# Kernel tuning notes

Hardware: AMD Instinct MI355X
Metric: run time of the kernel (lower is better)

The kernel has to match this reference:

```python
import jax, jax.numpy as jnp
import numpy as np

N_NODES, N_EDGES = 50000, 800000
NODE_D, EDGE_D, ST_D, HID_D = 64, 32, 32, 128


def _linear_params(key, fan_in, fan_out):
    k1, k2 = jax.random.split(key)
    lim = 1.0 / np.sqrt(fan_in)
    W = jax.random.uniform(k1, (fan_in, fan_out), jnp.float32, -lim, lim)
    b = jax.random.uniform(k2, (fan_out,), jnp.float32, -lim, lim)
    return W, b


def setup_inputs() -> dict:
    key = jax.random.key(0)
    ks = jax.random.split(key, 9)
    node_features = jax.random.normal(ks[0], (N_NODES, NODE_D), jnp.float32)
    edge_features = jax.random.normal(ks[1], (N_EDGES, EDGE_D), jnp.float32)
    spacetime_embeddings = jax.random.normal(ks[2], (N_NODES, ST_D), jnp.float32)
    edge_indices = jax.random.randint(ks[3], (N_EDGES, 2), 0, N_NODES, jnp.int64 if jax.config.jax_enable_x64 else jnp.int32)
    msg_in_d = 2 * NODE_D + EDGE_D + ST_D  # 192
    mW1, mb1 = _linear_params(ks[4], msg_in_d, HID_D)
    mW2, mb2 = _linear_params(ks[5], HID_D, HID_D)
    mW3, mb3 = _linear_params(ks[6], HID_D, NODE_D)
    uW1, ub1 = _linear_params(ks[7], NODE_D + ST_D, HID_D)
    uW2, ub2 = _linear_params(ks[8], HID_D, NODE_D)
    return dict(node_features=node_features, edge_features=edge_features,
                spacetime_embeddings=spacetime_embeddings,
                mW1=mW1, mb1=mb1, mW2=mW2, mb2=mb2, mW3=mW3, mb3=mb3,
                uW1=uW1, ub1=ub1, uW2=uW2, ub2=ub2,
                edge_indices=edge_indices)


def reference(node_features, edge_features, spacetime_embeddings,
              mW1, mb1, mW2, mb2, mW3, mb3, uW1, ub1, uW2, ub2,
              edge_indices):
    num_nodes = node_features.shape[0]
    src = edge_indices[:, 0]
    dst = edge_indices[:, 1]
    # gather + concat -> [E, 2*node_d + edge_d + st_d]
    msg_in = jnp.concatenate([node_features[src], node_features[dst],
                              edge_features, spacetime_embeddings[src]], axis=-1)
    h = jax.nn.relu(msg_in @ mW1 + mb1)
    h = jax.nn.relu(h @ mW2 + mb2)
    messages = h @ mW3 + mb3  # [E, node_d]
    aggregated = jax.ops.segment_sum(messages, dst, num_segments=num_nodes)  # scatter-add
    upd_in = jnp.concatenate([node_features, spacetime_embeddings], axis=-1)
    upd = jax.nn.relu(upd_in @ uW1 + ub1) @ uW2 + ub2
    return node_features + upd, aggregated
```

## Files before the change

### kernel.cpp

```cpp
#include <hip/hip_runtime.h>
#include <stdint.h>

typedef unsigned short u16t;
typedef unsigned int   u32t;
typedef __attribute__((ext_vector_type(8))) short frag8;
typedef __attribute__((ext_vector_type(4))) float fragc;

#define NN 50000
#define NE 800000
#define NB_EDGE 12500
#define NB_NODE 782

#define W1P 0
#define W2P 24576
#define W3P 40960
#define U1P 49152
#define U2P 61440
#define NFB_OFF 139264
#define STB_OFF (NFB_OFF + 6400000)

#define PB_PACK 34
#define PB_ZERO 3125
#define PB_NF   1563
#define PB_ST   782

__device__ __forceinline__ u16t f2bf(float f) {
    u32t x = __builtin_bit_cast(u32t, f);
    x = x + 0x7FFFu + ((x >> 16) & 1u);
    return (u16t)(x >> 16);
}

__device__ __forceinline__ u32t pack_bf2(float x, float y) {
#if __has_builtin(__builtin_amdgcn_cvt_pk_bf16_f32)
    typedef __attribute__((ext_vector_type(2))) __bf16 bfv2;
    bfv2 r = __builtin_amdgcn_cvt_pk_bf16_f32(x, y);
    return __builtin_bit_cast(u32t, r);
#else
    return (u32t)f2bf(x) | ((u32t)f2bf(y) << 16);
#endif
}

__device__ __forceinline__ void prepack_one(int t, const float* w1, const float* w2,
                                            const float* w3, const float* u1,
                                            const float* u2, u16t* out) {
    const float* src; u16t* dst; int id, K, N;
    if (t < 3072)      { id = t;        K = 192; N = 128; src = w1; dst = out + W1P; }
    else if (t < 5120) { id = t - 3072; K = 128; N = 128; src = w2; dst = out + W2P; }
    else if (t < 6144) { id = t - 5120; K = 128; N = 64;  src = w3; dst = out + W3P; }
    else if (t < 7680) { id = t - 6144; K = 96;  N = 128; src = u1; dst = out + U1P; }
    else if (t < 8704) { id = t - 7680; K = 128; N = 64;  src = u2; dst = out + U2P; }
    else return;
    int lane = id & 63;
    int fl   = id >> 6;
    int ksteps = K >> 5;
    int nb = fl / ksteps, ks = fl - nb * ksteps;
    int n  = nb * 16 + (lane & 15);
    int k0 = ks * 32 + (lane >> 4) * 8;
    const float* s = src + (size_t)k0 * N + n;
    uint4 v;
    v.x = pack_bf2(s[0],           s[(size_t)N]);
    v.y = pack_bf2(s[2*(size_t)N], s[3*(size_t)N]);
    v.z = pack_bf2(s[4*(size_t)N], s[5*(size_t)N]);
    v.w = pack_bf2(s[6*(size_t)N], s[7*(size_t)N]);
    *(uint4*)(dst + (size_t)id * 8) = v;
}

__global__ void prep_k(const float* __restrict__ w1, const float* __restrict__ w2,
                       const float* __restrict__ w3, const float* __restrict__ u1,
                       const float* __restrict__ u2, u16t* __restrict__ wp,
                       float4* __restrict__ out1v,
                       const float* __restrict__ nf, u16t* __restrict__ nfb,
                       const float* __restrict__ st, u16t* __restrict__ stb) {
    int b = blockIdx.x;
    if (b < PB_PACK) {
        prepack_one(b * 256 + threadIdx.x, w1, w2, w3, u1, u2, wp);
    } else if (b < PB_PACK + PB_ZERO) {
        int i = (b - PB_PACK) * 256 + threadIdx.x;
        if (i < NN * 16) out1v[i] = make_float4(0.f, 0.f, 0.f, 0.f);
    } else if (b < PB_PACK + PB_ZERO + PB_NF) {
        int i = ((b - PB_PACK - PB_ZERO) * 256 + threadIdx.x) * 8;
        if (i < NN * 64) {
            float4 a = *(const float4*)(nf + i);
            float4 c = *(const float4*)(nf + i + 4);
            uint4 v;
            v.x = pack_bf2(a.x, a.y); v.y = pack_bf2(a.z, a.w);
            v.z = pack_bf2(c.x, c.y); v.w = pack_bf2(c.z, c.w);
            *(uint4*)(nfb + i) = v;
        }
    } else {
        int i = ((b - PB_PACK - PB_ZERO - PB_NF) * 256 + threadIdx.x) * 8;
        if (i < NN * 32) {
            float4 a = *(const float4*)(st + i);
            float4 c = *(const float4*)(st + i + 4);
            uint4 v;
            v.x = pack_bf2(a.x, a.y); v.y = pack_bf2(a.z, a.w);
            v.z = pack_bf2(c.x, c.y); v.w = pack_bf2(c.z, c.w);
            *(uint4*)(stb + i) = v;
        }
    }
}

__global__ __launch_bounds__(256, 6)
void fused_k(const u16t* __restrict__ nfb, const u16t* __restrict__ stb,
             const float* __restrict__ nf, const float* __restrict__ ef,
             const float* __restrict__ b1, const float* __restrict__ b2,
             const float* __restrict__ b3, const float* __restrict__ ub1,
             const float* __restrict__ ub2, const int* __restrict__ eidx,
             const u16t* __restrict__ wp,
             float* __restrict__ out0, float* __restrict__ out1) {
    __shared__ __align__(16) u16t R[64 * 192];
    __shared__ int dstL[64];
    const int tid  = threadIdx.x;
    const int lane = tid & 63;
    const int wv   = tid >> 6;
    const int lr   = lane & 15;
    const int qd   = lane >> 4;
    const int sw   = lr & 7;

    if (blockIdx.x >= NB_EDGE) {
        const int n0  = (blockIdx.x - NB_EDGE) * 64;
        const int m16 = wv * 16;
        int nd  = n0 + m16 + lr;
        int ncl = nd < NN ? nd : NN - 1;

        fragc acc[8];
        #pragma unroll
        for (int n = 0; n < 8; n++) acc[n] = (fragc){0.f, 0.f, 0.f, 0.f};
        {
            const frag8* w = (const frag8*)(wp + U1P);
            #pragma unroll
            for (int ks = 0; ks < 3; ks++) {
                frag8 bfr;
                if (ks < 2) bfr = *(const frag8*)(nfb + (size_t)ncl * 64 + ks * 32 + qd * 8);
                else        bfr = *(const frag8*)(stb + (size_t)ncl * 32 + qd * 8);
                #pragma unroll
                for (int n = 0; n < 8; n++)
                    acc[n] = __builtin_amdgcn_mfma_f32_16x16x32_bf16(
                        w[(n * 3 + ks) * 64 + lane], bfr, acc[n], 0, 0, 0);
            }
        }
        #pragma unroll
        for (int n = 0; n < 8; n++) {
            float4 bq = *(const float4*)(ub1 + n * 16 + qd * 4);
            int cc = n * 2 + (qd >> 1);
            float v0 = acc[n][0] + bq.x; v0 = v0 > 0.f ? v0 : 0.f;
            float v1 = acc[n][1] + bq.y; v1 = v1 > 0.f ? v1 : 0.f;
            float v2 = acc[n][2] + bq.z; v2 = v2 > 0.f ? v2 : 0.f;
            float v3 = acc[n][3] + bq.w; v3 = v3 > 0.f ? v3 : 0.f;
            uint2 hw; hw.x = pack_bf2(v0, v1); hw.y = pack_bf2(v2, v3);
            *(uint2*)(R + (m16 + lr) * 128 + ((cc ^ sw) << 3) + (qd & 1) * 4) = hw;
        }
        fragc a2[4];
        #pragma unroll
        for (int n = 0; n < 4; n++) a2[n] = (fragc){0.f, 0.f, 0.f, 0.f};
        {
            const frag8* w = (const frag8*)(wp + U2P);
            #pragma unroll
            for (int ks = 0; ks < 4; ks++) {
                int c = ks * 4 + qd;
                frag8 a = *(const frag8*)(R + (m16 + lr) * 128 + ((c ^ sw) << 3));
                #pragma unroll
                for (int n = 0; n < 4; n++)
                    a2[n] = __builtin_amdgcn_mfma_f32_16x16x32_bf16(
                        a, w[(n * 4 + ks) * 64 + lane], a2[n], 0, 0, 0);
            }
        }
        #pragma unroll
        for (int n = 0; n < 4; n++) {
            float bs = ub2[n * 16 + lr];
            #pragma unroll
            for (int r = 0; r < 4; r++) {
                int nd2 = n0 + m16 + qd * 4 + r;
                if (nd2 < NN) {
                    int col = n * 16 + lr;
                    out0[(size_t)nd2 * 64 + col] = nf[(size_t)nd2 * 64 + col] + a2[n][r] + bs;
                }
            }
        }
        return;
    }

    const int e0  = blockIdx.x * 64;
    const int nb0 = 2 * wv, nb1 = 2 * wv + 1;

    {
        int el = tid >> 2, p = tid & 3;
        int e = e0 + el;
        int s = eidx[2 * e], d = eidx[2 * e + 1];
        const uint4* nsb = (const uint4*)(nfb + (size_t)s * 64);
        const uint4* ndb = (const uint4*)(nfb + (size_t)d * 64);
        const uint4* spb = (const uint4*)(stb + (size_t)s * 32);
        u16t* xr = R + el * 192;
        const int k = el & 7;
        #pragma unroll
        for (int g = p; g < 20; g += 4) {
            uint4 v; int c;
            if (g < 8)       { v = nsb[g];      c = g; }
            else if (g < 16) { v = ndb[g - 8];  c = g; }
            else             { v = spb[g - 16]; c = g + 4; }
            *(uint4*)(xr + ((c ^ k) << 3)) = v;
        }
        const float4* epf = (const float4*)(ef + (size_t)e * 32);
        #pragma unroll
        for (int h = p; h < 8; h += 4) {
            float4 v = epf[h];
            uint2 pk;
            pk.x = pack_bf2(v.x, v.y);
            pk.y = pack_bf2(v.z, v.w);
            int c = 16 + (h >> 1);
            *(uint2*)(xr + ((c ^ k) << 3) + (h & 1) * 4) = pk;
        }
    }
    if (tid < 64) dstL[tid] = eidx[2 * (e0 + tid) + 1];
    __syncthreads();

    fragc acc[2][4];
    #pragma unroll
    for (int i = 0; i < 2; i++)
        #pragma unroll
        for (int m = 0; m < 4; m++) acc[i][m] = (fragc){0.f, 0.f, 0.f, 0.f};
    {
        const frag8* w = (const frag8*)(wp + W1P);
        #pragma unroll
        for (int ks = 0; ks < 6; ks++) {
            frag8 w0 = w[(nb0 * 6 + ks) * 64 + lane];
            frag8 w1 = w[(nb1 * 6 + ks) * 64 + lane];
            int c = ks * 4 + qd;
            #pragma unroll
            for (int m = 0; m < 4; m++) {
                frag8 x = *(const frag8*)(R + (m * 16 + lr) * 192 + ((c ^ sw) << 3));
                acc[0][m] = __builtin_amdgcn_mfma_f32_16x16x32_bf16(w0, x, acc[0][m], 0, 0, 0);
                acc[1][m] = __builtin_amdgcn_mfma_f32_16x16x32_bf16(w1, x, acc[1][m], 0, 0, 0);
            }
        }
    }
    __syncthreads();
    #pragma unroll
    for (int i = 0; i < 2; i++) {
        int nb = nb0 + i;
        float4 bq = *(const float4*)(b1 + nb * 16 + qd * 4);
        int cc = nb * 2 + (qd >> 1);
        #pragma unroll
        for (int m = 0; m < 4; m++) {
            float v0 = acc[i][m][0] + bq.x; v0 = v0 > 0.f ? v0 : 0.f;
            float v1 = acc[i][m][1] + bq.y; v1 = v1 > 0.f ? v1 : 0.f;
            float v2 = acc[i][m][2] + bq.z; v2 = v2 > 0.f ? v2 : 0.f;
            float v3 = acc[i][m][3] + bq.w; v3 = v3 > 0.f ? v3 : 0.f;
            uint2 hw; hw.x = pack_bf2(v0, v1); hw.y = pack_bf2(v2, v3);
            *(uint2*)(R + (m * 16 + lr) * 128 + ((cc ^ sw) << 3) + (qd & 1) * 4) = hw;
        }
    }
    __syncthreads();

    #pragma unroll
    for (int i = 0; i < 2; i++)
        #pragma unroll
        for (int m = 0; m < 4; m++) acc[i][m] = (fragc){0.f, 0.f, 0.f, 0.f};
    {
        const frag8* w = (const frag8*)(wp + W2P);
        #pragma unroll
        for (int ks = 0; ks < 4; ks++) {
            frag8 w0 = w[(nb0 * 4 + ks) * 64 + lane];
            frag8 w1 = w[(nb1 * 4 + ks) * 64 + lane];
            int c = ks * 4 + qd;
            #pragma unroll
            for (int m = 0; m < 4; m++) {
                frag8 x = *(const frag8*)(R + (m * 16 + lr) * 128 + ((c ^ sw) << 3));
                acc[0][m] = __builtin_amdgcn_mfma_f32_16x16x32_bf16(w0, x, acc[0][m], 0, 0, 0);
                acc[1][m] = __builtin_amdgcn_mfma_f32_16x16x32_bf16(w1, x, acc[1][m], 0, 0, 0);
            }
        }
    }
    __syncthreads();
    #pragma unroll
    for (int i = 0; i < 2; i++) {
        int nb = nb0 + i;
        float4 bq = *(const float4*)(b2 + nb * 16 + qd * 4);
        int cc = nb * 2 + (qd >> 1);
        #pragma unroll
        for (int m = 0; m < 4; m++) {
            float v0 = acc[i][m][0] + bq.x; v0 = v0 > 0.f ? v0 : 0.f;
            float v1 = acc[i][m][1] + bq.y; v1 = v1 > 0.f ? v1 : 0.f;
            float v2 = acc[i][m][2] + bq.z; v2 = v2 > 0.f ? v2 : 0.f;
            float v3 = acc[i][m][3] + bq.w; v3 = v3 > 0.f ? v3 : 0.f;
            uint2 hw; hw.x = pack_bf2(v0, v1); hw.y = pack_bf2(v2, v3);
            *(uint2*)(R + (m * 16 + lr) * 128 + ((cc ^ sw) << 3) + (qd & 1) * 4) = hw;
        }
    }
    __syncthreads();

    fragc a3[4];
    #pragma unroll
    for (int m = 0; m < 4; m++) a3[m] = (fragc){0.f, 0.f, 0.f, 0.f};
    {
        const frag8* w = (const frag8*)(wp + W3P);
        #pragma unroll
        for (int ks = 0; ks < 4; ks++) {
            frag8 wf = w[(wv * 4 + ks) * 64 + lane];
            int c = ks * 4 + qd;
            #pragma unroll
            for (int m = 0; m < 4; m++) {
                frag8 a = *(const frag8*)(R + (m * 16 + lr) * 128 + ((c ^ sw) << 3));
                a3[m] = __builtin_amdgcn_mfma_f32_16x16x32_bf16(a, wf, a3[m], 0, 0, 0);
            }
        }
    }
    {
        float bs = b3[wv * 16 + lr];
        #pragma unroll
        for (int m = 0; m < 4; m++)
            #pragma unroll
            for (int r = 0; r < 4; r++) {
                int row = m * 16 + qd * 4 + r;
                atomicAdd(out1 + (size_t)dstL[row] * 64 + wv * 16 + lr,
                          a3[m][r] + bs);
            }
    }
}

extern "C" void kernel_launch(void* const* d_in, const int* in_sizes, int n_in,
                              void* d_out, int out_size, void* d_ws, size_t ws_size,
                              hipStream_t stream) {
    const float* nf  = (const float*)d_in[0];
    const float* ef  = (const float*)d_in[1];
    const float* st  = (const float*)d_in[2];
    const float* mW1 = (const float*)d_in[3];
    const float* mb1 = (const float*)d_in[4];
    const float* mW2 = (const float*)d_in[5];
    const float* mb2 = (const float*)d_in[6];
    const float* mW3 = (const float*)d_in[7];
    const float* mb3 = (const float*)d_in[8];
    const float* uW1 = (const float*)d_in[9];
    const float* ub1 = (const float*)d_in[10];
    const float* uW2 = (const float*)d_in[11];
    const float* ub2 = (const float*)d_in[12];
    const int*  eidx = (const int*)d_in[13];

    float* out0 = (float*)d_out;
    float* out1 = out0 + (size_t)NN * 64;
    char*  ws   = (char*)d_ws;
    u16t*  wp   = (u16t*)ws;
    u16t*  nfb  = (u16t*)(ws + NFB_OFF);
    u16t*  stb  = (u16t*)(ws + STB_OFF);

    prep_k<<<PB_PACK + PB_ZERO + PB_NF + PB_ST, 256, 0, stream>>>(
        mW1, mW2, mW3, uW1, uW2, wp, (float4*)out1, nf, nfb, st, stb);
    fused_k<<<NB_EDGE + NB_NODE, 256, 0, stream>>>(
        nfb, stb, nf, ef, mb1, mb2, mb3, ub1, ub2, eidx, wp, out0, out1);
}
```

Measured before the change: 364.9 us.

## Process two edge tiles per block and prefetch next tile's gathers into registers

Each edge block now handles 128 edges in two 64-edge iterations. While the MLP for the first tile runs, the gathered node, spacetime and edge features for the second tile are loaded into registers, then written to shared memory at the start of the next iteration. This is meant to hide gather latency behind MFMA work. In exchange, register pressure goes up (occupancy hint lowered from 6 to 5 blocks), there are half as many edge blocks, and an extra barrier is needed between iterations.

Result: slower. 461.5 us (+26.5%).

```diff
diff --git a/kernel.cpp b/kernel.cpp
--- a/kernel.cpp
+++ b/kernel.cpp
@@ -8,7 +8,7 @@
 
 #define NN 50000
 #define NE 800000
-#define NB_EDGE 12500
+#define NB_EDGE 6250
 #define NB_NODE 782
 
 #define W1P 0
@@ -100,7 +100,7 @@
     }
 }
 
-__global__ __launch_bounds__(256, 6)
+__global__ __launch_bounds__(256, 5)
 void fused_k(const u16t* __restrict__ nfb, const u16t* __restrict__ stb,
              const float* __restrict__ nf, const float* __restrict__ ef,
              const float* __restrict__ b1, const float* __restrict__ b2,
@@ -180,141 +180,162 @@
         return;
     }
 
-    const int e0  = blockIdx.x * 64;
+    const int e0  = blockIdx.x * 128;
+    const int el  = tid >> 2, p = tid & 3;
     const int nb0 = 2 * wv, nb1 = 2 * wv + 1;
 
-    {
-        int el = tid >> 2, p = tid & 3;
-        int e = e0 + el;
-        int s = eidx[2 * e], d = eidx[2 * e + 1];
+    uint4  gv[5];
+    float4 gf[2];
+    int    gdst;
+
+    auto LOADG = [&](int e) {
+        int2 sd = *(const int2*)(eidx + 2 * e);
+        int s = sd.x, d = sd.y;
+        gdst = d;
         const uint4* nsb = (const uint4*)(nfb + (size_t)s * 64);
         const uint4* ndb = (const uint4*)(nfb + (size_t)d * 64);
         const uint4* spb = (const uint4*)(stb + (size_t)s * 32);
+        #pragma unroll
+        for (int j = 0; j < 5; j++) {
+            int g = p + 4 * j;
+            gv[j] = (g < 8) ? nsb[g] : (g < 16 ? ndb[g - 8] : spb[g - 16]);
+        }
+        const float4* epf = (const float4*)(ef + (size_t)e * 32);
+        gf[0] = epf[p];
+        gf[1] = epf[p + 4];
+    };
+    auto WRITEG = [&]() {
         u16t* xr = R + el * 192;
         const int k = el & 7;
         #pragma unroll
-        for (int g = p; g < 20; g += 4) {
-            uint4 v; int c;
-            if (g < 8)       { v = nsb[g];      c = g; }
-            else if (g < 16) { v = ndb[g - 8];  c = g; }
-            else             { v = spb[g - 16]; c = g + 4; }
-            *(uint4*)(xr + ((c ^ k) << 3)) = v;
-        }
-        const float4* epf = (const float4*)(ef + (size_t)e * 32);
-        #pragma unroll
-        for (int h = p; h < 8; h += 4) {
-            float4 v = epf[h];
+        for (int j = 0; j < 5; j++) {
+            int g = p + 4 * j;
+            int c = (g < 16) ? g : g + 4;
+            *(uint4*)(xr + ((c ^ k) << 3)) = gv[j];
+        }
+        #pragma unroll
+        for (int q = 0; q < 2; q++) {
+            int h = p + 4 * q;
             uint2 pk;
-            pk.x = pack_bf2(v.x, v.y);
-            pk.y = pack_bf2(v.z, v.w);
+            pk.x = pack_bf2(gf[q].x, gf[q].y);
+            pk.y = pack_bf2(gf[q].z, gf[q].w);
             int c = 16 + (h >> 1);
             *(uint2*)(xr + ((c ^ k) << 3) + (h & 1) * 4) = pk;
         }
-    }
-    if (tid < 64) dstL[tid] = eidx[2 * (e0 + tid) + 1];
-    __syncthreads();
-
-    fragc acc[2][4];
+        if (p == 0) dstL[el] = gdst;
+    };
+
+    LOADG(e0 + el);
+
     #pragma unroll
-    for (int i = 0; i < 2; i++)
-        #pragma unroll
-        for (int m = 0; m < 4; m++) acc[i][m] = (fragc){0.f, 0.f, 0.f, 0.f};
-    {
-        const frag8* w = (const frag8*)(wp + W1P);
-        #pragma unroll
-        for (int ks = 0; ks < 6; ks++) {
-            frag8 w0 = w[(nb0 * 6 + ks) * 64 + lane];
-            frag8 w1 = w[(nb1 * 6 + ks) * 64 + lane];
-            int c = ks * 4 + qd;
+    for (int t = 0; t < 2; ++t) {
+        WRITEG();
+        __syncthreads();
+        if (t == 0) LOADG(e0 + 64 + el);
+
+        fragc acc[2][4];
+        #pragma unroll
+        for (int i = 0; i < 2; i++)
+            #pragma unroll
+            for (int m = 0; m < 4; m++) acc[i][m] = (fragc){0.f, 0.f, 0.f, 0.f};
+        {
+            const frag8* w = (const frag8*)(wp + W1P);
+            #pragma unroll
+            for (int ks = 0; ks < 6; ks++) {
+                frag8 w0 = w[(nb0 * 6 + ks) * 64 + lane];
+                frag8 w1 = w[(nb1 * 6 + ks) * 64 + lane];
+                int c = ks * 4 + qd;
+                #pragma unroll
+                for (int m = 0; m < 4; m++) {
+                    frag8 x = *(const frag8*)(R + (m * 16 + lr) * 192 + ((c ^ sw) << 3));
+                    acc[0][m] = __builtin_amdgcn_mfma_f32_16x16x32_bf16(w0, x, acc[0][m], 0, 0, 0);
+                    acc[1][m] = __builtin_amdgcn_mfma_f32_16x16x32_bf16(w1, x, acc[1][m], 0, 0, 0);
+                }
+            }
+        }
+        __syncthreads();
+        #pragma unroll
+        for (int i = 0; i < 2; i++) {
+            int nb = nb0 + i;
+            float4 bq = *(const float4*)(b1 + nb * 16 + qd * 4);
+            int cc = nb * 2 + (qd >> 1);
             #pragma unroll
             for (int m = 0; m < 4; m++) {
-                frag8 x = *(const frag8*)(R + (m * 16 + lr) * 192 + ((c ^ sw) << 3));
-                acc[0][m] = __builtin_amdgcn_mfma_f32_16x16x32_bf16(w0, x, acc[0][m], 0, 0, 0);
-                acc[1][m] = __builtin_amdgcn_mfma_f32_16x16x32_bf16(w1, x, acc[1][m], 0, 0, 0);
-            }
-        }
-    }
-    __syncthreads();
-    #pragma unroll
-    for (int i = 0; i < 2; i++) {
-        int nb = nb0 + i;
-        float4 bq = *(const float4*)(b1 + nb * 16 + qd * 4);
-        int cc = nb * 2 + (qd >> 1);
-        #pragma unroll
-        for (int m = 0; m < 4; m++) {
-            float v0 = acc[i][m][0] + bq.x; v0 = v0 > 0.f ? v0 : 0.f;
-            float v1 = acc[i][m][1] + bq.y; v1 = v1 > 0.f ? v1 : 0.f;
-            float v2 = acc[i][m][2] + bq.z; v2 = v2 > 0.f ? v2 : 0.f;
-            float v3 = acc[i][m][3] + bq.w; v3 = v3 > 0.f ? v3 : 0.f;
-            uint2 hw; hw.x = pack_bf2(v0, v1); hw.y = pack_bf2(v2, v3);
-            *(uint2*)(R + (m * 16 + lr) * 128 + ((cc ^ sw) << 3) + (qd & 1) * 4) = hw;
-        }
-    }
-    __syncthreads();
-
-    #pragma unroll
-    for (int i = 0; i < 2; i++)
-        #pragma unroll
-        for (int m = 0; m < 4; m++) acc[i][m] = (fragc){0.f, 0.f, 0.f, 0.f};
-    {
-        const frag8* w = (const frag8*)(wp + W2P);
-        #pragma unroll
-        for (int ks = 0; ks < 4; ks++) {
-            frag8 w0 = w[(nb0 * 4 + ks) * 64 + lane];
-            frag8 w1 = w[(nb1 * 4 + ks) * 64 + lane];
-            int c = ks * 4 + qd;
+                float v0 = acc[i][m][0] + bq.x; v0 = v0 > 0.f ? v0 : 0.f;
+                float v1 = acc[i][m][1] + bq.y; v1 = v1 > 0.f ? v1 : 0.f;
+                float v2 = acc[i][m][2] + bq.z; v2 = v2 > 0.f ? v2 : 0.f;
+                float v3 = acc[i][m][3] + bq.w; v3 = v3 > 0.f ? v3 : 0.f;
+                uint2 hw; hw.x = pack_bf2(v0, v1); hw.y = pack_bf2(v2, v3);
+                *(uint2*)(R + (m * 16 + lr) * 128 + ((cc ^ sw) << 3) + (qd & 1) * 4) = hw;
+            }
+        }
+        __syncthreads();
+
+        #pragma unroll
+        for (int i = 0; i < 2; i++)
+            #pragma unroll
+            for (int m = 0; m < 4; m++) acc[i][m] = (fragc){0.f, 0.f, 0.f, 0.f};
+        {
+            const frag8* w = (const frag8*)(wp + W2P);
+            #pragma unroll
+            for (int ks = 0; ks < 4; ks++) {
+                frag8 w0 = w[(nb0 * 4 + ks) * 64 + lane];
+                frag8 w1 = w[(nb1 * 4 + ks) * 64 + lane];
+                int c = ks * 4 + qd;
+                #pragma unroll
+                for (int m = 0; m < 4; m++) {
+                    frag8 x = *(const frag8*)(R + (m * 16 + lr) * 128 + ((c ^ sw) << 3));
+                    acc[0][m] = __builtin_amdgcn_mfma_f32_16x16x32_bf16(w0, x, acc[0][m], 0, 0, 0);
+                    acc[1][m] = __builtin_amdgcn_mfma_f32_16x16x32_bf16(w1, x, acc[1][m], 0, 0, 0);
+                }
+            }
+        }
+        __syncthreads();
+        #pragma unroll
+        for (int i = 0; i < 2; i++) {
+            int nb = nb0 + i;
+            float4 bq = *(const float4*)(b2 + nb * 16 + qd * 4);
+            int cc = nb * 2 + (qd >> 1);
             #pragma unroll
             for (int m = 0; m < 4; m++) {
-                frag8 x = *(const frag8*)(R + (m * 16 + lr) * 128 + ((c ^ sw) << 3));
-                acc[0][m] = __builtin_amdgcn_mfma_f32_16x16x32_bf16(w0, x, acc[0][m], 0, 0, 0);
-                acc[1][m] = __builtin_amdgcn_mfma_f32_16x16x32_bf16(w1, x, acc[1][m], 0, 0, 0);
-            }
-        }
-    }
-    __syncthreads();
-    #pragma unroll
-    for (int i = 0; i < 2; i++) {
-        int nb = nb0 + i;
-        float4 bq = *(const float4*)(b2 + nb * 16 + qd * 4);
-        int cc = nb * 2 + (qd >> 1);
-        #pragma unroll
-        for (int m = 0; m < 4; m++) {
-            float v0 = acc[i][m][0] + bq.x; v0 = v0 > 0.f ? v0 : 0.f;
-            float v1 = acc[i][m][1] + bq.y; v1 = v1 > 0.f ? v1 : 0.f;
-            float v2 = acc[i][m][2] + bq.z; v2 = v2 > 0.f ? v2 : 0.f;
-            float v3 = acc[i][m][3] + bq.w; v3 = v3 > 0.f ? v3 : 0.f;
-            uint2 hw; hw.x = pack_bf2(v0, v1); hw.y = pack_bf2(v2, v3);
-            *(uint2*)(R + (m * 16 + lr) * 128 + ((cc ^ sw) << 3) + (qd & 1) * 4) = hw;
-        }
-    }
-    __syncthreads();
-
-    fragc a3[4];
-    #pragma unroll
-    for (int m = 0; m < 4; m++) a3[m] = (fragc){0.f, 0.f, 0.f, 0.f};
-    {
-        const frag8* w = (const frag8*)(wp + W3P);
-        #pragma unroll
-        for (int ks = 0; ks < 4; ks++) {
-            frag8 wf = w[(wv * 4 + ks) * 64 + lane];
-            int c = ks * 4 + qd;
-            #pragma unroll
-            for (int m = 0; m < 4; m++) {
-                frag8 a = *(const frag8*)(R + (m * 16 + lr) * 128 + ((c ^ sw) << 3));
-                a3[m] = __builtin_amdgcn_mfma_f32_16x16x32_bf16(a, wf, a3[m], 0, 0, 0);
-            }
-        }
-    }
-    {
-        float bs = b3[wv * 16 + lr];
-        #pragma unroll
-        for (int m = 0; m < 4; m++)
-            #pragma unroll
-            for (int r = 0; r < 4; r++) {
-                int row = m * 16 + qd * 4 + r;
-                atomicAdd(out1 + (size_t)dstL[row] * 64 + wv * 16 + lr,
-                          a3[m][r] + bs);
-            }
+                float v0 = acc[i][m][0] + bq.x; v0 = v0 > 0.f ? v0 : 0.f;
+                float v1 = acc[i][m][1] + bq.y; v1 = v1 > 0.f ? v1 : 0.f;
+                float v2 = acc[i][m][2] + bq.z; v2 = v2 > 0.f ? v2 : 0.f;
+                float v3 = acc[i][m][3] + bq.w; v3 = v3 > 0.f ? v3 : 0.f;
+                uint2 hw; hw.x = pack_bf2(v0, v1); hw.y = pack_bf2(v2, v3);
+                *(uint2*)(R + (m * 16 + lr) * 128 + ((cc ^ sw) << 3) + (qd & 1) * 4) = hw;
+            }
+        }
+        __syncthreads();
+
+        fragc a3[4];
+        #pragma unroll
+        for (int m = 0; m < 4; m++) a3[m] = (fragc){0.f, 0.f, 0.f, 0.f};
+        {
+            const frag8* w = (const frag8*)(wp + W3P);
+            #pragma unroll
+            for (int ks = 0; ks < 4; ks++) {
+                frag8 wf = w[(wv * 4 + ks) * 64 + lane];
+                int c = ks * 4 + qd;
+                #pragma unroll
+                for (int m = 0; m < 4; m++) {
+                    frag8 a = *(const frag8*)(R + (m * 16 + lr) * 128 + ((c ^ sw) << 3));
+                    a3[m] = __builtin_amdgcn_mfma_f32_16x16x32_bf16(a, wf, a3[m], 0, 0, 0);
+                }
+            }
+        }
+        {
+            float bs = b3[wv * 16 + lr];
+            #pragma unroll
+            for (int m = 0; m < 4; m++)
+                #pragma unroll
+                for (int r = 0; r < 4; r++) {
+                    int row = m * 16 + qd * 4 + r;
+                    atomicAdd(out1 + (size_t)dstL[row] * 64 + wv * 16 + lr,
+                              a3[m][r] + bs);
+                }
+        }
+        if (t == 0) __syncthreads();
     }
 }
 
```

## Halve fused block to 32 edges with 2 waves and raise MFMA priority

Applied to the files above, without the earlier changes.

Each fused block now uses 128 threads (2 waves) on 32 edges or 32 nodes instead of 256 threads on 64, so the grid doubles. Each wave now covers 4 output column blocks over 2 row tiles rather than 2 over 4, which changes how weight fragments are reused against LDS activations. The edge gather now writes dstL from the gather threads. s_setprio is raised around the MFMA loops so matrix work is favoured over the memory-heavy waves. The smaller LDS footprint per block should allow more resident blocks and better latency hiding, but each wave loads more weight fragments per activation read and uses more accumulator registers.

Result: slower. 437.6 us (+19.9%).

```diff
diff --git a/kernel.cpp b/kernel.cpp
--- a/kernel.cpp
+++ b/kernel.cpp
@@ -8,8 +8,8 @@
 
 #define NN 50000
 #define NE 800000
-#define NB_EDGE 12500
-#define NB_NODE 782
+#define NB_EDGE 25000
+#define NB_NODE 1563
 
 #define W1P 0
 #define W2P 24576
@@ -100,7 +100,7 @@
     }
 }
 
-__global__ __launch_bounds__(256, 6)
+__global__ __launch_bounds__(128, 6)
 void fused_k(const u16t* __restrict__ nfb, const u16t* __restrict__ stb,
              const float* __restrict__ nf, const float* __restrict__ ef,
              const float* __restrict__ b1, const float* __restrict__ b2,
@@ -108,8 +108,8 @@
              const float* __restrict__ ub2, const int* __restrict__ eidx,
              const u16t* __restrict__ wp,
              float* __restrict__ out0, float* __restrict__ out1) {
-    __shared__ __align__(16) u16t R[64 * 192];
-    __shared__ int dstL[64];
+    __shared__ __align__(16) u16t R[32 * 192];
+    __shared__ int dstL[32];
     const int tid  = threadIdx.x;
     const int lane = tid & 63;
     const int wv   = tid >> 6;
@@ -118,7 +118,7 @@
     const int sw   = lr & 7;
 
     if (blockIdx.x >= NB_EDGE) {
-        const int n0  = (blockIdx.x - NB_EDGE) * 64;
+        const int n0  = (blockIdx.x - NB_EDGE) * 32;
         const int m16 = wv * 16;
         int nd  = n0 + m16 + lr;
         int ncl = nd < NN ? nd : NN - 1;
@@ -128,6 +128,7 @@
         for (int n = 0; n < 8; n++) acc[n] = (fragc){0.f, 0.f, 0.f, 0.f};
         {
             const frag8* w = (const frag8*)(wp + U1P);
+            __builtin_amdgcn_s_setprio(1);
             #pragma unroll
             for (int ks = 0; ks < 3; ks++) {
                 frag8 bfr;
@@ -138,6 +139,7 @@
                     acc[n] = __builtin_amdgcn_mfma_f32_16x16x32_bf16(
                         w[(n * 3 + ks) * 64 + lane], bfr, acc[n], 0, 0, 0);
             }
+            __builtin_amdgcn_s_setprio(0);
         }
         #pragma unroll
         for (int n = 0; n < 8; n++) {
@@ -155,6 +157,7 @@
         for (int n = 0; n < 4; n++) a2[n] = (fragc){0.f, 0.f, 0.f, 0.f};
         {
             const frag8* w = (const frag8*)(wp + U2P);
+            __builtin_amdgcn_s_setprio(1);
             #pragma unroll
             for (int ks = 0; ks < 4; ks++) {
                 int c = ks * 4 + qd;
@@ -164,6 +167,7 @@
                     a2[n] = __builtin_amdgcn_mfma_f32_16x16x32_bf16(
                         a, w[(n * 4 + ks) * 64 + lane], a2[n], 0, 0, 0);
             }
+            __builtin_amdgcn_s_setprio(0);
         }
         #pragma unroll
         for (int n = 0; n < 4; n++) {
@@ -180,8 +184,7 @@
         return;
     }
 
-    const int e0  = blockIdx.x * 64;
-    const int nb0 = 2 * wv, nb1 = 2 * wv + 1;
+    const int e0 = blockIdx.x * 32;
 
     {
         int el = tid >> 2, p = tid & 3;
@@ -210,38 +213,43 @@
             int c = 16 + (h >> 1);
             *(uint2*)(xr + ((c ^ k) << 3) + (h & 1) * 4) = pk;
         }
-    }
-    if (tid < 64) dstL[tid] = eidx[2 * (e0 + tid) + 1];
-    __syncthreads();
-
-    fragc acc[2][4];
-    #pragma unroll
-    for (int i = 0; i < 2; i++)
-        #pragma unroll
-        for (int m = 0; m < 4; m++) acc[i][m] = (fragc){0.f, 0.f, 0.f, 0.f};
+        if (p == 0) dstL[el] = d;
+    }
+    __syncthreads();
+
+    fragc acc[4][2];
+    #pragma unroll
+    for (int i = 0; i < 4; i++)
+        #pragma unroll
+        for (int m = 0; m < 2; m++) acc[i][m] = (fragc){0.f, 0.f, 0.f, 0.f};
     {
         const frag8* w = (const frag8*)(wp + W1P);
+        __builtin_amdgcn_s_setprio(1);
         #pragma unroll
         for (int ks = 0; ks < 6; ks++) {
-            frag8 w0 = w[(nb0 * 6 + ks) * 64 + lane];
-            frag8 w1 = w[(nb1 * 6 + ks) * 64 + lane];
+            frag8 wf[4];
+            #pragma unroll
+            for (int i = 0; i < 4; i++)
+                wf[i] = w[((4 * wv + i) * 6 + ks) * 64 + lane];
             int c = ks * 4 + qd;
             #pragma unroll
-            for (int m = 0; m < 4; m++) {
+            for (int m = 0; m < 2; m++) {
                 frag8 x = *(const frag8*)(R + (m * 16 + lr) * 192 + ((c ^ sw) << 3));
-                acc[0][m] = __builtin_amdgcn_mfma_f32_16x16x32_bf16(w0, x, acc[0][m], 0, 0, 0);
-                acc[1][m] = __builtin_amdgcn_mfma_f32_16x16x32_bf16(w1, x, acc[1][m], 0, 0, 0);
-            }
-        }
-    }
-    __syncthreads();
-    #pragma unroll
-    for (int i = 0; i < 2; i++) {
-        int nb = nb0 + i;
+                #pragma unroll
+                for (int i = 0; i < 4; i++)
+                    acc[i][m] = __builtin_amdgcn_mfma_f32_16x16x32_bf16(wf[i], x, acc[i][m], 0, 0, 0);
+            }
+        }
+        __builtin_amdgcn_s_setprio(0);
+    }
+    __syncthreads();
+    #pragma unroll
+    for (int i = 0; i < 4; i++) {
+        int nb = 4 * wv + i;
         float4 bq = *(const float4*)(b1 + nb * 16 + qd * 4);
         int cc = nb * 2 + (qd >> 1);
         #pragma unroll
-        for (int m = 0; m < 4; m++) {
+        for (int m = 0; m < 2; m++) {
             float v0 = acc[i][m][0] + bq.x; v0 = v0 > 0.f ? v0 : 0.f;
             float v1 = acc[i][m][1] + bq.y; v1 = v1 > 0.f ? v1 : 0.f;
             float v2 = acc[i][m][2] + bq.z; v2 = v2 > 0.f ? v2 : 0.f;
@@ -253,32 +261,37 @@
     __syncthreads();
 
     #pragma unroll
-    for (int i = 0; i < 2; i++)
-        #pragma unroll
-        for (int m = 0; m < 4; m++) acc[i][m] = (fragc){0.f, 0.f, 0.f, 0.f};
+    for (int i = 0; i < 4; i++)
+        #pragma unroll
+        for (int m = 0; m < 2; m++) acc[i][m] = (fragc){0.f, 0.f, 0.f, 0.f};
     {
         const frag8* w = (const frag8*)(wp + W2P);
+        __builtin_amdgcn_s_setprio(1);
         #pragma unroll
         for (int ks = 0; ks < 4; ks++) {
-            frag8 w0 = w[(nb0 * 4 + ks) * 64 + lane];
-            frag8 w1 = w[(nb1 * 4 + ks) * 64 + lane];
+            frag8 wf[4];
+            #pragma unroll
+            for (int i = 0; i < 4; i++)
+                wf[i] = w[((4 * wv + i) * 4 + ks) * 64 + lane];
             int c = ks * 4 + qd;
             #pragma unroll
-            for (int m = 0; m < 4; m++) {
+            for (int m = 0; m < 2; m++) {
                 frag8 x = *(const frag8*)(R + (m * 16 + lr) * 128 + ((c ^ sw) << 3));
-                acc[0][m] = __builtin_amdgcn_mfma_f32_16x16x32_bf16(w0, x, acc[0][m], 0, 0, 0);
-                acc[1][m] = __builtin_amdgcn_mfma_f32_16x16x32_bf16(w1, x, acc[1][m], 0, 0, 0);
-            }
-        }
-    }
-    __syncthreads();
-    #pragma unroll
-    for (int i = 0; i < 2; i++) {
-        int nb = nb0 + i;
+                #pragma unroll
+                for (int i = 0; i < 4; i++)
+                    acc[i][m] = __builtin_amdgcn_mfma_f32_16x16x32_bf16(wf[i], x, acc[i][m], 0, 0, 0);
+            }
+        }
+        __builtin_amdgcn_s_setprio(0);
+    }
+    __syncthreads();
+    #pragma unroll
+    for (int i = 0; i < 4; i++) {
+        int nb = 4 * wv + i;
         float4 bq = *(const float4*)(b2 + nb * 16 + qd * 4);
         int cc = nb * 2 + (qd >> 1);
         #pragma unroll
-        for (int m = 0; m < 4; m++) {
+        for (int m = 0; m < 2; m++) {
             float v0 = acc[i][m][0] + bq.x; v0 = v0 > 0.f ? v0 : 0.f;
             float v1 = acc[i][m][1] + bq.y; v1 = v1 > 0.f ? v1 : 0.f;
             float v2 = acc[i][m][2] + bq.z; v2 = v2 > 0.f ? v2 : 0.f;
@@ -289,31 +302,42 @@
     }
     __syncthreads();
 
-    fragc a3[4];
-    #pragma unroll
-    for (int m = 0; m < 4; m++) a3[m] = (fragc){0.f, 0.f, 0.f, 0.f};
+    fragc a3[2][2];
+    #pragma unroll
+    for (int i = 0; i < 2; i++)
+        #pragma unroll
+        for (int m = 0; m < 2; m++) a3[i][m] = (fragc){0.f, 0.f, 0.f, 0.f};
     {
         const frag8* w = (const frag8*)(wp + W3P);
+        __builtin_amdgcn_s_setprio(1);
         #pragma unroll
         for (int ks = 0; ks < 4; ks++) {
-            frag8 wf = w[(wv * 4 + ks) * 64 + lane];
+            frag8 wf[2];
+            #pragma unroll
+            for (int i = 0; i < 2; i++)
+                wf[i] = w[((2 * wv + i) * 4 + ks) * 64 + lane];
             int c = ks * 4 + qd;
             #pragma unroll
-            for (int m = 0; m < 4; m++) {
+            for (int m = 0; m < 2; m++) {
                 frag8 a = *(const frag8*)(R + (m * 16 + lr) * 128 + ((c ^ sw) << 3));
-                a3[m] = __builtin_amdgcn_mfma_f32_16x16x32_bf16(a, wf, a3[m], 0, 0, 0);
-            }
-        }
-    }
-    {
-        float bs = b3[wv * 16 + lr];
-        #pragma unroll
-        for (int m = 0; m < 4; m++)
+                #pragma unroll
+                for (int i = 0; i < 2; i++)
+                    a3[i][m] = __builtin_amdgcn_mfma_f32_16x16x32_bf16(a, wf[i], a3[i][m], 0, 0, 0);
+            }
+        }
+        __builtin_amdgcn_s_setprio(0);
+    }
+    #pragma unroll
+    for (int i = 0; i < 2; i++) {
+        int nb = 2 * wv + i;
+        float bs = b3[nb * 16 + lr];
+        #pragma unroll
+        for (int m = 0; m < 2; m++)
             #pragma unroll
             for (int r = 0; r < 4; r++) {
                 int row = m * 16 + qd * 4 + r;
-                atomicAdd(out1 + (size_t)dstL[row] * 64 + wv * 16 + lr,
-                          a3[m][r] + bs);
+                atomicAdd(out1 + (size_t)dstL[row] * 64 + nb * 16 + lr,
+                          a3[i][m][r] + bs);
             }
     }
 }
@@ -345,6 +369,6 @@
 
     prep_k<<<PB_PACK + PB_ZERO + PB_NF + PB_ST, 256, 0, stream>>>(
         mW1, mW2, mW3, uW1, uW2, wp, (float4*)out1, nf, nfb, st, stb);
-    fused_k<<<NB_EDGE + NB_NODE, 256, 0, stream>>>(
+    fused_k<<<NB_EDGE + NB_NODE, 128, 0, stream>>>(
         nfb, stb, nf, ef, mb1, mb2, mb3, ub1, ub2, eidx, wp, out0, out1);
 }
```
